# Kernel tuning notes

Measured on AMD Instinct MI355X. Metric: run time of the kernel, lower is better.

The kernel has to match this reference:

```python
import jax, jax.numpy as jnp
import numpy as np

QMAX = 127.0

def fake_quant(x):
    # per-tensor symmetric int8 fake quantize-dequantize (QAT)
    s = jnp.maximum(jnp.max(jnp.abs(x)) / QMAX, 1e-8)
    q = jnp.clip(jnp.round(x / s), -QMAX, QMAX) * s
    return x + jax.lax.stop_gradient(q - x)  # STE

def qlinear(x, w, b):
    # x already fake-quantized by caller (input_quantizer); weights fake-quantized here
    return jnp.einsum('btc,oc->bto', x, fake_quant(w)) + b

def layer_norm(x, g, b, eps=1e-5):
    m = jnp.mean(x, axis=-1, keepdims=True)
    v = jnp.var(x, axis=-1, keepdims=True)
    return (x - m) * jax.lax.rsqrt(v + eps) * g + b

def setup_inputs() -> dict:
    key = jax.random.key(0)
    ks = jax.random.split(key, 8)
    B, T, C, I = 8, 512, 1024, 4096
    sd = 0.02
    return {
        'hidden_states': jax.random.normal(ks[0], (B, T, C), jnp.float32),
        'attention_mask': jnp.ones((B, T), jnp.float32),
        'ln1_g': jnp.ones((C,), jnp.float32), 'ln1_b': jnp.zeros((C,), jnp.float32),
        'ln2_g': jnp.ones((C,), jnp.float32), 'ln2_b': jnp.zeros((C,), jnp.float32),
        'w_qkv': sd * jax.random.normal(ks[1], (3 * C, C), jnp.float32),
        'b_qkv': jnp.zeros((3 * C,), jnp.float32),
        'w_out': sd * jax.random.normal(ks[2], (C, C), jnp.float32),
        'b_out': jnp.zeros((C,), jnp.float32),
        'w1': sd * jax.random.normal(ks[3], (I, C), jnp.float32),
        'b1': jnp.zeros((I,), jnp.float32),
        'w2': sd * jax.random.normal(ks[4], (C, I), jnp.float32),
        'b2': jnp.zeros((C,), jnp.float32),
    }

def reference(hidden_states, attention_mask, ln1_g, ln1_b, ln2_g, ln2_b,
              w_qkv, b_qkv, w_out, b_out, w1, b1, w2, b2):
    B, T, C = hidden_states.shape
    H = 16
    Dh = C // H
    scale = Dh ** -0.5

    # --- attention branch (pre-norm) ---
    x = layer_norm(hidden_states, ln1_g, ln1_b)
    qkv = qlinear(fake_quant(x), w_qkv, b_qkv)            # [B,T,3C]
    qkv = qkv.reshape(B, T, 3, H, Dh).transpose(2, 0, 3, 1, 4)
    q, k, v = qkv[0], qkv[1], qkv[2]                       # [B,H,T,Dh]
    scores = jnp.einsum('bhqd,bhkd->bhqk', q, k) * scale
    ext = (1.0 - attention_mask)[:, None, None, :] * -10000.0
    scores = scores + ext
    attn = jax.nn.softmax(scores, axis=-1)
    out = jnp.einsum('bhqk,bhkd->bhqd', attn, v)
    out = out.transpose(0, 2, 1, 3).reshape(B, T, C)
    attn_out = qlinear(fake_quant(out), w_out, b_out)
    h = hidden_states + attn_out

    # --- MLP branch (pre-norm) ---
    x = layer_norm(h, ln2_g, ln2_b)
    x = qlinear(fake_quant(x), w1, b1)
    x = jax.nn.gelu(x, approximate=False)
    x = qlinear(fake_quant(x), w2, b2)
    return h + x
```

## Files before the change

kernel.cpp:

```cpp
#include <hip/hip_runtime.h>

typedef __attribute__((ext_vector_type(8))) short bf16x8;
typedef __attribute__((ext_vector_type(4))) float f32x4;
typedef __attribute__((ext_vector_type(4))) int i32x4;
typedef unsigned short u16;
typedef unsigned int u32;

#define B_ 8
#define T_ 512
#define C_ 1024
#define I_ 4096
#define H_ 16
#define Dh_ 64
#define BT (B_*T_)
#define NH (B_*H_)

__device__ __forceinline__ float bf2f(u16 u) {
  return __uint_as_float(((u32)u) << 16);
}
__device__ __forceinline__ u16 f2bf(float f) {
  u32 u = __float_as_uint(f);
  u32 r = u + 0x7FFFu + ((u >> 16) & 1u);
  return (u16)(r >> 16);
}
__device__ __forceinline__ float wredMax(float v) {
#pragma unroll
  for (int o = 32; o; o >>= 1) v = fmaxf(v, __shfl_xor(v, o));
  return v;
}
__device__ __forceinline__ float wredSum(float v) {
#pragma unroll
  for (int o = 32; o; o >>= 1) v += __shfl_xor(v, o);
  return v;
}
__device__ __forceinline__ void slotAtomicMax(u32* arr, int bid, float bm) {
  u32 b = __float_as_uint(bm);
  volatile u32* p = arr + ((bid & 63) << 4);
  if (b > *p) atomicMax((u32*)p, b);
}
__device__ __forceinline__ float slotMax(const u32* __restrict__ arr) {
  float m = 0.f;
#pragma unroll
  for (int i = 0; i < 64; ++i) m = fmaxf(m, __uint_as_float(arr[i << 4]));
  return m;
}
__device__ __forceinline__ void gload16(const void* g, void* l) {
  __builtin_amdgcn_global_load_lds((const __attribute__((address_space(1))) void*)g,
                                   (__attribute__((address_space(3))) void*)l, 16, 0, 0);
}
__device__ __forceinline__ int qi(float v, float inv) {
  return (int)fminf(fmaxf(rintf(v * inv), -127.f), 127.f);
}
__device__ __forceinline__ float gelu1(float v) {
  float x2 = v * v;
  float e = __expf(v * fmaf(-0.0713548755f, x2, -1.5957691216f));
  return v * __builtin_amdgcn_rcpf(1.0f + e);
}

__global__ void k_init(u32* s) {
  int i = blockIdx.x * 256 + threadIdx.x;
  if (i < 8192) s[i] = 0u;
}

__global__ __launch_bounds__(256) void k_absmax4(
    const float* __restrict__ p0, int n0,
    const float* __restrict__ p1, int n1,
    const float* __restrict__ p2, int n2,
    const float* __restrict__ p3, int n3,
    u32* __restrict__ sc) {
  int stride = gridDim.x * blockDim.x;
  int gid = blockIdx.x * blockDim.x + threadIdx.x;
  float m0 = 0.f, m1 = 0.f, m2 = 0.f, m3 = 0.f;
  for (int i = gid; i < n0; i += stride) {
    float4 v = ((const float4*)p0)[i];
    m0 = fmaxf(m0, fmaxf(fmaxf(fabsf(v.x), fabsf(v.y)), fmaxf(fabsf(v.z), fabsf(v.w))));
  }
  for (int i = gid; i < n1; i += stride) {
    float4 v = ((const float4*)p1)[i];
    m1 = fmaxf(m1, fmaxf(fmaxf(fabsf(v.x), fabsf(v.y)), fmaxf(fabsf(v.z), fabsf(v.w))));
  }
  for (int i = gid; i < n2; i += stride) {
    float4 v = ((const float4*)p2)[i];
    m2 = fmaxf(m2, fmaxf(fmaxf(fabsf(v.x), fabsf(v.y)), fmaxf(fabsf(v.z), fabsf(v.w))));
  }
  for (int i = gid; i < n3; i += stride) {
    float4 v = ((const float4*)p3)[i];
    m3 = fmaxf(m3, fmaxf(fmaxf(fabsf(v.x), fabsf(v.y)), fmaxf(fabsf(v.z), fabsf(v.w))));
  }
  m0 = wredMax(m0); m1 = wredMax(m1); m2 = wredMax(m2); m3 = wredMax(m3);
  __shared__ float red[4][4];
  int wid = threadIdx.x >> 6, lane = threadIdx.x & 63;
  if (lane == 0) { red[wid][0] = m0; red[wid][1] = m1; red[wid][2] = m2; red[wid][3] = m3; }
  __syncthreads();
  if (threadIdx.x < 4) {
    int j = threadIdx.x;
    float bm = fmaxf(fmaxf(red[0][j], red[1][j]), fmaxf(red[2][j], red[3][j]));
    slotAtomicMax(sc + j * 1024, blockIdx.x, bm);
  }
}

__global__ __launch_bounds__(256) void k_quant4(
    const float* __restrict__ p0, signed char* __restrict__ q0, int n0,
    const float* __restrict__ p1, signed char* __restrict__ q1, int n1,
    const float* __restrict__ p2, signed char* __restrict__ q2, int n2,
    const float* __restrict__ p3, signed char* __restrict__ q3, int n3,
    const u32* __restrict__ sc) {
  int stride = gridDim.x * blockDim.x;
  int gid = blockIdx.x * blockDim.x + threadIdx.x;
#define QLOOP(p, q, n, slot)                                                        \
  {                                                                                 \
    float s = fmaxf(slotMax(sc + slot * 1024) * (1.0f / 127.0f), 1e-8f);            \
    float inv = 1.0f / s;                                                           \
    for (int i = gid; i < n; i += stride) {                                         \
      float4 v = ((const float4*)p)[i];                                             \
      u32 pk = (u32)(qi(v.x, inv) & 255) | ((u32)(qi(v.y, inv) & 255) << 8) |       \
               ((u32)(qi(v.z, inv) & 255) << 16) | ((u32)(qi(v.w, inv) & 255) << 24); \
      ((u32*)q)[i] = pk;                                                            \
    }                                                                               \
  }
  QLOOP(p0, q0, n0, 0)
  QLOOP(p1, q1, n1, 1)
  QLOOP(p2, q2, n2, 2)
  QLOOP(p3, q3, n3, 3)
#undef QLOOP
}

__global__ __launch_bounds__(256) void k_quant_b8(const u16* __restrict__ x, signed char* __restrict__ q,
                                                  int n8, const u32* __restrict__ arr) {
  float s = fmaxf(slotMax(arr) * (1.0f / 127.0f), 1e-8f);
  float inv = 1.0f / s;
  int stride = gridDim.x * blockDim.x;
  for (int i = blockIdx.x * blockDim.x + threadIdx.x; i < n8; i += stride) {
    uint4 d = ((const uint4*)x)[i];
    u16* e = (u16*)&d;
    uint2 o;
    o.x = (u32)(qi(bf2f(e[0]), inv) & 255) | ((u32)(qi(bf2f(e[1]), inv) & 255) << 8) |
          ((u32)(qi(bf2f(e[2]), inv) & 255) << 16) | ((u32)(qi(bf2f(e[3]), inv) & 255) << 24);
    o.y = (u32)(qi(bf2f(e[4]), inv) & 255) | ((u32)(qi(bf2f(e[5]), inv) & 255) << 8) |
          ((u32)(qi(bf2f(e[6]), inv) & 255) << 16) | ((u32)(qi(bf2f(e[7]), inv) & 255) << 24);
    ((uint2*)q)[i] = o;
  }
}

__global__ __launch_bounds__(256) void k_ln(const float* __restrict__ x, const float* __restrict__ g,
                                            const float* __restrict__ b, u16* __restrict__ y,
                                            u32* __restrict__ arr) {
  int row = blockIdx.x;
  int t = threadIdx.x;
  float4 v = ((const float4*)(x + (long)row * C_))[t];
  float s1 = v.x + v.y + v.z + v.w;
  float s2 = v.x * v.x + v.y * v.y + v.z * v.z + v.w * v.w;
  s1 = wredSum(s1);
  s2 = wredSum(s2);
  __shared__ float red[8];
  int wid = t >> 6, lane = t & 63;
  if (lane == 0) { red[wid] = s1; red[4 + wid] = s2; }
  __syncthreads();
  s1 = red[0] + red[1] + red[2] + red[3];
  s2 = red[4] + red[5] + red[6] + red[7];
  float mean = s1 * (1.0f / C_);
  float var = s2 * (1.0f / C_) - mean * mean;
  float inv = rsqrtf(var + 1e-5f);
  float4 gv = ((const float4*)g)[t];
  float4 bv = ((const float4*)b)[t];
  float4 o;
  o.x = (v.x - mean) * inv * gv.x + bv.x;
  o.y = (v.y - mean) * inv * gv.y + bv.y;
  o.z = (v.z - mean) * inv * gv.z + bv.z;
  o.w = (v.w - mean) * inv * gv.w + bv.w;
  ushort4 ob;
  ob.x = f2bf(o.x); ob.y = f2bf(o.y); ob.z = f2bf(o.z); ob.w = f2bf(o.w);
  ((ushort4*)(y + (long)row * C_))[t] = ob;
  float m = fmaxf(fmaxf(fabsf(o.x), fabsf(o.y)), fmaxf(fabsf(o.z), fabsf(o.w)));
  m = wredMax(m);
  __syncthreads();
  if (lane == 0) red[wid] = m;
  __syncthreads();
  if (t == 0) {
    float bm = fmaxf(fmaxf(red[0], red[1]), fmaxf(red[2], red[3]));
    slotAtomicMax(arr, row, bm);
  }
}

__global__ __launch_bounds__(256, 1) void k_attn(
    const u16* __restrict__ qkv, const float* __restrict__ mask,
    u16* __restrict__ O, u32* __restrict__ amax) {
  __shared__ u16 Ke[512 * 64];
  __shared__ u16 Vt[64 * 512];
  __shared__ u16 Pl[4 * 64 * 40];
  __shared__ float extl[512];
  __shared__ float redm[4];
  const int tid = threadIdx.x;
  const int w = tid >> 6, l = tid & 63;
  const int head = blockIdx.x;
  const int chunk = blockIdx.y;
  const int b = head >> 4, h = head & 15;
  const long rowbase = (long)(b * 512) * (3 * C_);

  {
    const u16* Kg = qkv + rowbase + C_ + h * 64;
    int lr8 = l >> 3;
    int ls = (l & 7) ^ lr8;
    const long koff = (long)lr8 * (3 * C_) + ls * 8;
#pragma unroll
    for (int i = 0; i < 16; ++i) {
      int r0 = w * 128 + i * 8;
      gload16(Kg + (long)r0 * (3 * C_) + koff, &Ke[r0 * 64]);
    }
  }
  {
    const u16* Vg = qkv + rowbase + 2 * C_ + h * 64;
    int kvl = tid & 31;
    int d0 = (tid >> 5) * 8;
#pragma unroll 4
    for (int i = 0; i < 16; ++i) {
      int kv = i * 32 + kvl;
      uint4 t4 = *(const uint4*)(Vg + (long)kv * (3 * C_) + d0);
      u16* tv = (u16*)&t4;
      int slot = kv >> 3, within = kv & 7;
#pragma unroll
      for (int j = 0; j < 8; ++j) {
        int d = d0 + j;
        Vt[d * 512 + ((slot ^ (d & 7)) << 3) + within] = tv[j];
      }
    }
  }
  {
    const float* mb = mask + b * 512;
    extl[tid] = (1.0f - mb[tid]) * -10000.0f;
    extl[tid + 256] = (1.0f - mb[tid + 256]) * -10000.0f;
  }
  const int qbase = chunk * 256 + w * 64;
  bf16x8 qf[4][2];
  {
    const u16* Qg = qkv + rowbase + h * 64;
#pragma unroll
    for (int qt = 0; qt < 4; ++qt)
#pragma unroll
      for (int dc = 0; dc < 2; ++dc)
        qf[qt][dc] = *(const bf16x8*)(Qg + (long)(qbase + qt * 16 + (l & 15)) * (3 * C_) + dc * 32 + (l >> 4) * 8);
  }
  __syncthreads();

  f32x4 oacc[4][4];
  float mrun[4], lrun[4];
#pragma unroll
  for (int qt = 0; qt < 4; ++qt) { mrun[qt] = -3.0e38f; lrun[qt] = 0.f; }
#pragma unroll
  for (int dt = 0; dt < 4; ++dt)
#pragma unroll
    for (int qt = 0; qt < 4; ++qt) oacc[dt][qt] = (f32x4){0.f, 0.f, 0.f, 0.f};

  u16* Pw = &Pl[w * 64 * 40];

  for (int ks = 0; ks < 16; ++ks) {
    bf16x8 kf[2][2];
#pragma unroll
    for (int kvt = 0; kvt < 2; ++kvt) {
      int kv = ks * 32 + kvt * 16 + (l & 15);
#pragma unroll
      for (int dc = 0; dc < 2; ++dc) {
        int phys = (dc * 4 + (l >> 4)) ^ (kv & 7);
        kf[kvt][dc] = *(const bf16x8*)&Ke[kv * 64 + phys * 8];
      }
    }
    f32x4 sacc[2][4];
#pragma unroll
    for (int kvt = 0; kvt < 2; ++kvt)
#pragma unroll
      for (int qt = 0; qt < 4; ++qt) {
        f32x4 a = (f32x4){0.f, 0.f, 0.f, 0.f};
        a = __builtin_amdgcn_mfma_f32_16x16x32_bf16(kf[kvt][0], qf[qt][0], a, 0, 0, 0);
        a = __builtin_amdgcn_mfma_f32_16x16x32_bf16(kf[kvt][1], qf[qt][1], a, 0, 0, 0);
        sacc[kvt][qt] = a;
      }
#pragma unroll
    for (int kvt = 0; kvt < 2; ++kvt) {
      f32x4 ev = *(const f32x4*)&extl[ks * 32 + kvt * 16 + (l >> 4) * 4];
#pragma unroll
      for (int qt = 0; qt < 4; ++qt)
#pragma unroll
        for (int r = 0; r < 4; ++r)
          sacc[kvt][qt][r] = fmaf(sacc[kvt][qt][r], 0.125f, ev[r]);
    }
#pragma unroll
    for (int qt = 0; qt < 4; ++qt) {
      float pm = sacc[0][qt][0];
#pragma unroll
      for (int r = 1; r < 4; ++r) pm = fmaxf(pm, sacc[0][qt][r]);
#pragma unroll
      for (int r = 0; r < 4; ++r) pm = fmaxf(pm, sacc[1][qt][r]);
      pm = fmaxf(pm, __shfl_xor(pm, 16));
      pm = fmaxf(pm, __shfl_xor(pm, 32));
      float mnew = fmaxf(mrun[qt], pm);
      float f = __expf(mrun[qt] - mnew);
      mrun[qt] = mnew;
      float lsum = 0.f;
#pragma unroll
      for (int kvt = 0; kvt < 2; ++kvt)
#pragma unroll
        for (int r = 0; r < 4; ++r) {
          float p = __expf(sacc[kvt][qt][r] - mnew);
          sacc[kvt][qt][r] = p;
          lsum += p;
        }
      lsum += __shfl_xor(lsum, 16);
      lsum += __shfl_xor(lsum, 32);
      lrun[qt] = lrun[qt] * f + lsum;
#pragma unroll
      for (int dt = 0; dt < 4; ++dt)
#pragma unroll
        for (int r = 0; r < 4; ++r) oacc[dt][qt][r] *= f;
#pragma unroll
      for (int kvt = 0; kvt < 2; ++kvt) {
        u32 p01 = (u32)f2bf(sacc[kvt][qt][0]) | ((u32)f2bf(sacc[kvt][qt][1]) << 16);
        u32 p23 = (u32)f2bf(sacc[kvt][qt][2]) | ((u32)f2bf(sacc[kvt][qt][3]) << 16);
        u16* pr = Pw + (qt * 16 + (l & 15)) * 40 + kvt * 16 + (l >> 4) * 4;
        *(u32*)pr = p01;
        *(u32*)(pr + 2) = p23;
      }
    }
    bf16x8 vf[4], pf[4];
#pragma unroll
    for (int dt = 0; dt < 4; ++dt) {
      int d = dt * 16 + (l & 15);
      int phys = (ks * 4 + (l >> 4)) ^ (d & 7);
      vf[dt] = *(const bf16x8*)&Vt[d * 512 + phys * 8];
    }
#pragma unroll
    for (int qt = 0; qt < 4; ++qt)
      pf[qt] = *(const bf16x8*)(Pw + (qt * 16 + (l & 15)) * 40 + (l >> 4) * 8);
#pragma unroll
    for (int dt = 0; dt < 4; ++dt)
#pragma unroll
      for (int qt = 0; qt < 4; ++qt)
        oacc[dt][qt] = __builtin_amdgcn_mfma_f32_16x16x32_bf16(vf[dt], pf[qt], oacc[dt][qt], 0, 0, 0);
  }

  float lmax = 0.f;
  u16* Ob = O + (long)(b * 512 + qbase) * C_ + h * 64;
#pragma unroll
  for (int qt = 0; qt < 4; ++qt) {
    float inv = 1.0f / lrun[qt];
    long qoff = (long)(qt * 16 + (l & 15)) * C_;
#pragma unroll
    for (int dt = 0; dt < 4; ++dt) {
      int d = dt * 16 + (l >> 4) * 4;
      float v0 = oacc[dt][qt][0] * inv;
      float v1 = oacc[dt][qt][1] * inv;
      float v2 = oacc[dt][qt][2] * inv;
      float v3 = oacc[dt][qt][3] * inv;
      lmax = fmaxf(fmaxf(lmax, fmaxf(fabsf(v0), fabsf(v1))), fmaxf(fabsf(v2), fabsf(v3)));
      u32 a01 = (u32)f2bf(v0) | ((u32)f2bf(v1) << 16);
      u32 a23 = (u32)f2bf(v2) | ((u32)f2bf(v3) << 16);
      *(u32*)(Ob + qoff + d) = a01;
      *(u32*)(Ob + qoff + d + 2) = a23;
    }
  }
  lmax = wredMax(lmax);
  if (l == 0) redm[w] = lmax;
  __syncthreads();
  if (tid == 0)
    slotAtomicMax(amax, blockIdx.x * 2 + blockIdx.y,
                  fmaxf(fmaxf(redm[0], redm[1]), fmaxf(redm[2], redm[3])));
}

template <int BM, int BN, int EPI, bool SWZ>
__global__ __launch_bounds__(256) void k_gemmq(
    const signed char* __restrict__ A, int lda,
    const signed char* __restrict__ Bm, int ldb,
    const float* __restrict__ bias,
    void* __restrict__ Cp, int ldc,
    int M, int N, int K,
    const float* __restrict__ resid,
    u32* __restrict__ amaxOut,
    const u32* __restrict__ amaxA, const u32* __restrict__ amaxB) {
  constexpr int BK = 128;
  constexpr int MF = (BM / 2) / 16;
  constexpr int NF = (BN / 2) / 16;
  constexpr int NLD = BM / 32 + BN / 32;
  __shared__ __align__(16) signed char As[2][BM * BK];
  __shared__ __align__(16) signed char Bs[2][BN * BK];
  const int tid = threadIdx.x;
  const int wid = tid >> 6, lane = tid & 63;
  const int wr = wid >> 1, wc = wid & 1;

  float sa = fmaxf(slotMax(amaxA) * (1.0f / 127.0f), 1e-8f);
  float sb = fmaxf(slotMax(amaxB) * (1.0f / 127.0f), 1e-8f);
  const float sAB = sa * sb;

  int bx = blockIdx.x, by = blockIdx.y;
  if (SWZ) {
    int gx = gridDim.x;
    int nwg = gx * gridDim.y;
    int bid = by * gx + bx;
    int cpx = nwg >> 3;
    int swz = (bid & 7) * cpx + (bid >> 3);
    bx = swz % gx;
    by = swz / gx;
  }

  const signed char* Ab = A + (long)by * BM * lda;
  const signed char* Bb = Bm + (long)bx * BN * ldb;

  i32x4 acc[MF][NF];
#pragma unroll
  for (int m = 0; m < MF; m++)
#pragma unroll
    for (int n = 0; n < NF; n++) acc[m][n] = (i32x4){0, 0, 0, 0};

  const int lr = lane & 15;
  const int l8 = lane >> 3;
  const int s8 = (lane & 7) ^ l8;
  const long aoff = (long)l8 * lda + s8 * 16;
  const long boff = (long)l8 * ldb + s8 * 16;

  auto stageAB = [&](int buf, int k0) {
#pragma unroll
    for (int i = 0; i < BM / 32; ++i) {
      int R0 = wid * (BM / 4) + i * 8;
      gload16(Ab + (long)R0 * lda + k0 + aoff, &As[buf][R0 * BK]);
    }
#pragma unroll
    for (int i = 0; i < BN / 32; ++i) {
      int R0 = wid * (BN / 4) + i * 8;
      gload16(Bb + (long)R0 * ldb + k0 + boff, &Bs[buf][R0 * BK]);
    }
  };

  auto waitCounted = [&]() {
    if constexpr (NLD == 8) {
      asm volatile("s_waitcnt vmcnt(8)" ::: "memory");
    } else if constexpr (NLD == 6) {
      asm volatile("s_waitcnt vmcnt(6)" ::: "memory");
    } else {
      asm volatile("s_waitcnt vmcnt(4)" ::: "memory");
    }
  };

  auto computeK = [&](int buf) {
#pragma unroll
    for (int kk = 0; kk < 2; ++kk) {
      const int sl = (kk << 2) + (lane >> 4);
      const int sf = (sl ^ (lr & 7)) << 4;
      i32x4 af[MF], bfr[NF];
#pragma unroll
      for (int m = 0; m < MF; m++)
        af[m] = *(const i32x4*)&As[buf][(wr * (BM / 2) + m * 16 + lr) * BK + sf];
#pragma unroll
      for (int n = 0; n < NF; n++)
        bfr[n] = *(const i32x4*)&Bs[buf][(wc * (BN / 2) + n * 16 + lr) * BK + sf];
      __builtin_amdgcn_s_setprio(1);
#pragma unroll
      for (int m = 0; m < MF; m++)
#pragma unroll
        for (int n = 0; n < NF; n++)
          acc[m][n] = __builtin_amdgcn_mfma_i32_16x16x64_i8(af[m], bfr[n], acc[m][n], 0, 0, 0);
      __builtin_amdgcn_s_setprio(0);
    }
  };

  const int nt = K / BK;
  stageAB(0, 0);
  int cur = 0;
  for (int t = 0; t < nt; ++t) {
    if (t + 1 < nt) {
      stageAB(cur ^ 1, (t + 1) * BK);
      waitCounted();
    } else {
      asm volatile("s_waitcnt vmcnt(0)" ::: "memory");
    }
    __builtin_amdgcn_s_barrier();
    computeK(cur);
    if (t + 1 < nt)
      __builtin_amdgcn_s_barrier();
    cur ^= 1;
  }

  const int rowBase = by * BM + wr * (BM / 2);
  const int colBase = bx * BN + wc * (BN / 2);
  float lmax = 0.f;
#pragma unroll
  for (int m = 0; m < MF; m++) {
    int row0 = rowBase + m * 16 + (lane >> 4) * 4;
#pragma unroll
    for (int n = 0; n < NF; n++) {
      int col = colBase + n * 16 + lr;
      float bs = bias[col];
#pragma unroll
      for (int j = 0; j < 4; j++) {
        int row = row0 + j;
        long idx = (long)row * ldc + col;
        float v = (float)acc[m][n][j] * sAB;
        if (EPI == 0) {
          ((u16*)Cp)[idx] = f2bf(v + bs);
        } else if (EPI == 1) {
          ((float*)Cp)[idx] = v + bs + resid[idx];
        } else if (EPI == 2) {
          v = gelu1(v + bs);
          lmax = fmaxf(fmaxf(lmax, v), 0.0f - v);
          ((u16*)Cp)[idx] = f2bf(v);
        } else if (EPI == 3) {
          ((float*)Cp)[idx] = v + bs + resid[idx];
        }
      }
    }
  }
  if (EPI == 2) {
    __shared__ float redm[4];
    float wm = wredMax(lmax);
    if (lane == 0) redm[wid] = wm;
    __syncthreads();
    if (tid == 0) {
      float bm = fmaxf(fmaxf(redm[0], redm[1]), fmaxf(redm[2], redm[3]));
      slotAtomicMax(amaxOut, blockIdx.y * gridDim.x + blockIdx.x, bm);
    }
  }
}

__global__ __launch_bounds__(512, 1) void k_gemmq8(
    const signed char* __restrict__ A, int lda,
    const signed char* __restrict__ Bm, int ldb,
    const float* __restrict__ bias,
    u16* __restrict__ Cp, int ldc,
    int K,
    u32* __restrict__ amaxOut,
    const u32* __restrict__ amaxA, const u32* __restrict__ amaxB) {
  __shared__ __align__(16) signed char As[2][256 * 128];
  __shared__ __align__(16) signed char Bs[2][256 * 128];
  const int tid = threadIdx.x;
  const int wid = tid >> 6, lane = tid & 63;
  const int wr = wid >> 2, wc = wid & 3;
  const int lr = lane & 15;

  float sa = fmaxf(slotMax(amaxA) * (1.0f / 127.0f), 1e-8f);
  float sb = fmaxf(slotMax(amaxB) * (1.0f / 127.0f), 1e-8f);
  const float sAB = sa * sb;

  int bx = blockIdx.x, by = blockIdx.y;
  {
    int bid = by * 16 + bx;
    int swz = (bid & 7) * 32 + (bid >> 3);
    bx = swz & 15;
    by = swz >> 4;
  }
  const signed char* Ab = A + (long)by * 256 * lda;
  const signed char* Bb = Bm + (long)bx * 256 * ldb;

  i32x4 acc[8][4];
#pragma unroll
  for (int m = 0; m < 8; m++)
#pragma unroll
    for (int n = 0; n < 4; n++) acc[m][n] = (i32x4){0, 0, 0, 0};

  const int l8 = lane >> 3;
  const int s8 = (lane & 7) ^ l8;
  const long aoff = (long)l8 * lda + s8 * 16;
  const long boff = (long)l8 * ldb + s8 * 16;

  auto stageHalf = [&](int buf, int kt, int h) {
    int k0 = kt * 128;
    if (h < 2) {
      int R0 = h * 128 + wid * 16;
      gload16(Ab + (long)R0 * lda + k0 + aoff, &As[buf][R0 * 128]);
      gload16(Ab + (long)(R0 + 8) * lda + k0 + aoff, &As[buf][(R0 + 8) * 128]);
    } else {
      int R0 = (h - 2) * 128 + wid * 16;
      gload16(Bb + (long)R0 * ldb + k0 + boff, &Bs[buf][R0 * 128]);
      gload16(Bb + (long)(R0 + 8) * ldb + k0 + boff, &Bs[buf][(R0 + 8) * 128]);
    }
  };

  const int nt = K / 128;
#define PHASE(BUF, Q, STAGESTMT)                                                   \
  {                                                                                \
    constexpr int mh = (Q) & 1, ks = (Q) >> 1;                                     \
    const int slotl = ks * 4 + (lane >> 4);                                        \
    i32x4 af[4], bfr[4];                                                           \
    _Pragma("unroll") for (int i = 0; i < 4; ++i) {                                \
      int row = wr * 128 + (mh * 4 + i) * 16 + lr;                                 \
      af[i] = *(const i32x4*)&As[BUF][row * 128 + ((slotl ^ (row & 7)) << 4)];     \
    }                                                                              \
    _Pragma("unroll") for (int n = 0; n < 4; ++n) {                                \
      int row = wc * 64 + n * 16 + lr;                                             \
      bfr[n] = *(const i32x4*)&Bs[BUF][row * 128 + ((slotl ^ (row & 7)) << 4)];    \
    }                                                                              \
    STAGESTMT;                                                                     \
    __builtin_amdgcn_s_barrier();                                                  \
    __builtin_amdgcn_s_setprio(1);                                                 \
    _Pragma("unroll") for (int i = 0; i < 4; ++i)                                  \
      _Pragma("unroll") for (int n = 0; n < 4; ++n)                                \
        acc[mh * 4 + i][n] =                                                       \
            __builtin_amdgcn_mfma_i32_16x16x64_i8(af[i], bfr[n], acc[mh * 4 + i][n], 0, 0, 0); \
    __builtin_amdgcn_s_setprio(0);                                                 \
    __builtin_amdgcn_s_barrier();                                                  \
  }

#pragma unroll
  for (int h = 0; h < 4; ++h) stageHalf(0, 0, h);

  for (int it = 0; it < nt / 2; ++it) {
    const int kt0 = 2 * it;
    const bool st2 = (kt0 + 2) < nt;
    asm volatile("s_waitcnt vmcnt(0)" ::: "memory");
    __builtin_amdgcn_s_barrier();
    PHASE(0, 0, { stageHalf(1, kt0 + 1, 0); stageHalf(1, kt0 + 1, 1); })
    PHASE(0, 1, { stageHalf(1, kt0 + 1, 2); stageHalf(1, kt0 + 1, 3); })
    PHASE(0, 2, {})
    PHASE(0, 3, {})
    asm volatile("s_waitcnt vmcnt(0)" ::: "memory");
    __builtin_amdgcn_s_barrier();
    PHASE(1, 0, { if (st2) { stageHalf(0, kt0 + 2, 0); stageHalf(0, kt0 + 2, 1); } })
    PHASE(1, 1, { if (st2) { stageHalf(0, kt0 + 2, 2); stageHalf(0, kt0 + 2, 3); } })
    PHASE(1, 2, {})
    PHASE(1, 3, {})
  }
#undef PHASE

  const int rowBase = by * 256 + wr * 128;
  const int colBase = bx * 256 + wc * 64;
  float lmax = 0.f;
#pragma unroll
  for (int m = 0; m < 8; m++) {
    int row0 = rowBase + m * 16 + (lane >> 4) * 4;
#pragma unroll
    for (int n = 0; n < 4; n++) {
      int col = colBase + n * 16 + lr;
      float bs = bias[col];
#pragma unroll
      for (int j = 0; j < 4; j++) {
        long idx = (long)(row0 + j) * ldc + col;
        float v = gelu1((float)acc[m][n][j] * sAB + bs);
        lmax = fmaxf(fmaxf(lmax, v), 0.0f - v);
        Cp[idx] = f2bf(v);
      }
    }
  }
  {
    __shared__ float redm[8];
    float wm = wredMax(lmax);
    if (lane == 0) redm[wid] = wm;
    __syncthreads();
    if (tid == 0) {
      float bm = redm[0];
#pragma unroll
      for (int i = 1; i < 8; ++i) bm = fmaxf(bm, redm[i]);
      slotAtomicMax(amaxOut, blockIdx.y * gridDim.x + blockIdx.x, bm);
    }
  }
}

extern "C" void kernel_launch(void* const* d_in, const int* in_sizes, int n_in,
                              void* d_out, int out_size, void* d_ws, size_t ws_size,
                              hipStream_t stream) {
  const float* hidden = (const float*)d_in[0];
  const float* mask = (const float*)d_in[1];
  const float* ln1g = (const float*)d_in[2];
  const float* ln1b = (const float*)d_in[3];
  const float* ln2g = (const float*)d_in[4];
  const float* ln2b = (const float*)d_in[5];
  const float* w_qkv = (const float*)d_in[6];
  const float* b_qkv = (const float*)d_in[7];
  const float* w_out = (const float*)d_in[8];
  const float* b_out = (const float*)d_in[9];
  const float* w1 = (const float*)d_in[10];
  const float* b1 = (const float*)d_in[11];
  const float* w2 = (const float*)d_in[12];
  const float* b2 = (const float*)d_in[13];

  char* ws = (char*)d_ws;
  u32* sc = (u32*)ws;
  const long MB = 1024 * 1024;
  signed char* wq_qkv = (signed char*)(ws + 1 * MB);
  signed char* wq_out = (signed char*)(ws + 4 * MB);
  signed char* wq_w1  = (signed char*)(ws + 6 * MB);
  signed char* wq_w2  = (signed char*)(ws + 10 * MB);
  signed char* xq     = (signed char*)(ws + 14 * MB);
  u16* x1             = (u16*)(ws + 18 * MB);
  signed char* Oq     = (signed char*)(ws + 26 * MB);
  u16* O              = (u16*)(ws + 30 * MB);
  u16* qkv            = (u16*)(ws + 38 * MB);
  float* hbuf         = (float*)(ws + 62 * MB);
  u16* y1             = (u16*)(ws + 78 * MB);
  signed char* y1q    = (signed char*)(ws + 110 * MB);

  k_init<<<32, 256, 0, stream>>>(sc);

  k_absmax4<<<512, 256, 0, stream>>>(
      w_qkv, 3 * C_ * C_ / 4, w_out, C_ * C_ / 4, w1, I_ * C_ / 4, w2, C_ * I_ / 4, sc);
  k_quant4<<<512, 256, 0, stream>>>(
      w_qkv, wq_qkv, 3 * C_ * C_ / 4, w_out, wq_out, C_ * C_ / 4,
      w1, wq_w1, I_ * C_ / 4, w2, wq_w2, C_ * I_ / 4, sc);

  k_ln<<<BT, 256, 0, stream>>>(hidden, ln1g, ln1b, x1, sc + 4 * 1024);
  k_quant_b8<<<512, 256, 0, stream>>>(x1, xq, BT * C_ / 8, sc + 4 * 1024);

  k_gemmq<128, 128, 0, true><<<dim3(24, 32), 256, 0, stream>>>(
      xq, C_, wq_qkv, C_, b_qkv, qkv, 3 * C_,
      BT, 3 * C_, C_, nullptr, nullptr, sc + 4 * 1024, sc + 0 * 1024);

  k_attn<<<dim3(NH, 2), 256, 0, stream>>>(qkv, mask, O, sc + 5 * 1024);
  k_quant_b8<<<512, 256, 0, stream>>>(O, Oq, BT * C_ / 8, sc + 5 * 1024);

  k_gemmq<64, 64, 1, true><<<dim3(16, 64), 256, 0, stream>>>(
      Oq, C_, wq_out, C_, b_out, hbuf, C_,
      BT, C_, C_, hidden, nullptr, sc + 5 * 1024, sc + 1 * 1024);

  k_ln<<<BT, 256, 0, stream>>>(hbuf, ln2g, ln2b, x1, sc + 6 * 1024);
  k_quant_b8<<<512, 256, 0, stream>>>(x1, xq, BT * C_ / 8, sc + 6 * 1024);

  k_gemmq8<<<dim3(16, 16), 512, 0, stream>>>(
      xq, C_, wq_w1, C_, b1, y1, I_, C_,
      sc + 7 * 1024, sc + 6 * 1024, sc + 2 * 1024);
  k_quant_b8<<<512, 256, 0, stream>>>(y1, y1q, BT * I_ / 8, sc + 7 * 1024);

  k_gemmq<64, 64, 3, true><<<dim3(16, 64), 256, 0, stream>>>(
      y1q, I_, wq_w2, I_, b2, d_out, C_,
      BT, C_, I_, hbuf, nullptr, sc + 7 * 1024, sc + 3 * 1024);
}
```

Measured before the change: 244.8 us.

## Reorder int8 GEMM pipeline with partial vmcnt waits and interleaved half-tile staging

Restructures the int8 MFMA GEMM main loop so loads for the next K-tile are issued in a different order (A-top, B-left, B-right, A-bottom) across the four phases of each tile. It also waits with partial vmcnt counts instead of draining all loads. The second M-half can start once only its needed A rows and B data have arrived, which overlaps more global load latency with compute. The trade-offs are a runtime buffer index instead of fixed buffers, and correctness that depends on the vmcnt counts matching the number of issued loads.

```diff
diff --git a/kernel.cpp b/kernel.cpp
--- a/kernel.cpp
+++ b/kernel.cpp
@@ -572,13 +572,12 @@
   };
 
   const int nt = K / 128;
-#define PHASE(BUF, Q, STAGESTMT)                                                   \
+#define PHASE(BUF, MH, KS, STAGESTMT)                                              \
   {                                                                                \
-    constexpr int mh = (Q) & 1, ks = (Q) >> 1;                                     \
-    const int slotl = ks * 4 + (lane >> 4);                                        \
+    const int slotl = (KS) * 4 + (lane >> 4);                                      \
     i32x4 af[4], bfr[4];                                                           \
     _Pragma("unroll") for (int i = 0; i < 4; ++i) {                                \
-      int row = wr * 128 + (mh * 4 + i) * 16 + lr;                                 \
+      int row = wr * 128 + ((MH) * 4 + i) * 16 + lr;                               \
       af[i] = *(const i32x4*)&As[BUF][row * 128 + ((slotl ^ (row & 7)) << 4)];     \
     }                                                                              \
     _Pragma("unroll") for (int n = 0; n < 4; ++n) {                                \
@@ -590,30 +589,35 @@
     __builtin_amdgcn_s_setprio(1);                                                 \
     _Pragma("unroll") for (int i = 0; i < 4; ++i)                                  \
       _Pragma("unroll") for (int n = 0; n < 4; ++n)                                \
-        acc[mh * 4 + i][n] =                                                       \
-            __builtin_amdgcn_mfma_i32_16x16x64_i8(af[i], bfr[n], acc[mh * 4 + i][n], 0, 0, 0); \
+        acc[(MH) * 4 + i][n] =                                                     \
+            __builtin_amdgcn_mfma_i32_16x16x64_i8(af[i], bfr[n], acc[(MH) * 4 + i][n], 0, 0, 0); \
     __builtin_amdgcn_s_setprio(0);                                                 \
     __builtin_amdgcn_s_barrier();                                                  \
   }
 
-#pragma unroll
-  for (int h = 0; h < 4; ++h) stageHalf(0, 0, h);
-
-  for (int it = 0; it < nt / 2; ++it) {
-    const int kt0 = 2 * it;
-    const bool st2 = (kt0 + 2) < nt;
-    asm volatile("s_waitcnt vmcnt(0)" ::: "memory");
+  stageHalf(0, 0, 0);
+  stageHalf(0, 0, 2);
+  stageHalf(0, 0, 3);
+  stageHalf(0, 0, 1);
+
+  int cur = 0;
+  for (int t = 0; t < nt; ++t) {
+    const bool stg = (t + 1 < nt);
+    const int nb = cur ^ 1;
+    const int tn = t + 1;
+    asm volatile("s_waitcnt vmcnt(2)" ::: "memory");
     __builtin_amdgcn_s_barrier();
-    PHASE(0, 0, { stageHalf(1, kt0 + 1, 0); stageHalf(1, kt0 + 1, 1); })
-    PHASE(0, 1, { stageHalf(1, kt0 + 1, 2); stageHalf(1, kt0 + 1, 3); })
-    PHASE(0, 2, {})
-    PHASE(0, 3, {})
-    asm volatile("s_waitcnt vmcnt(0)" ::: "memory");
+    PHASE(cur, 0, 0, { if (stg) stageHalf(nb, tn, 0); })
+    PHASE(cur, 0, 1, { if (stg) stageHalf(nb, tn, 2); })
+    if (stg) {
+      asm volatile("s_waitcnt vmcnt(4)" ::: "memory");
+    } else {
+      asm volatile("s_waitcnt vmcnt(0)" ::: "memory");
+    }
     __builtin_amdgcn_s_barrier();
-    PHASE(1, 0, { if (st2) { stageHalf(0, kt0 + 2, 0); stageHalf(0, kt0 + 2, 1); } })
-    PHASE(1, 1, { if (st2) { stageHalf(0, kt0 + 2, 2); stageHalf(0, kt0 + 2, 3); } })
-    PHASE(1, 2, {})
-    PHASE(1, 3, {})
+    PHASE(cur, 1, 0, { if (stg) stageHalf(nb, tn, 3); })
+    PHASE(cur, 1, 1, { if (stg) stageHalf(nb, tn, 1); })
+    cur = nb;
   }
 #undef PHASE
 
```

Result: no change. 241.6 us (-1.3%).
